# Performance work log

Measured on AMD Instinct MI355X. Metric: run time of the kernel, lower is better.

Reference implementation:

```python
import jax, jax.numpy as jnp
import numpy as np

N = 100000          # nodes
E = 800000          # directed edges (before self-loops)
IN_C = 3
HID = 48            # out_channels per head
HEADS = 4
NUM_LAYERS = 3
NEG_SLOPE = 0.2     # PyG GATv2Conv default negative_slope


def setup_inputs() -> dict:
    key = jax.random.key(0)
    ks = iter(jax.random.split(key, 64))
    inp = {}
    inp["x"] = jax.random.normal(next(ks), (N, IN_C), dtype=jnp.float32)
    inp["edge_index"] = jax.random.randint(next(ks), (2, E), 0, N, dtype=jnp.int32)
    dins = [IN_C] + [HID] * (NUM_LAYERS - 1)
    for l, din in enumerate(dins):
        s = 1.0 / np.sqrt(din)
        inp[f"Wl{l}"] = (jax.random.normal(next(ks), (din, HEADS * HID)) * s).astype(jnp.float32)
        inp[f"bl{l}"] = jnp.zeros((HEADS * HID,), jnp.float32)
        inp[f"Wr{l}"] = (jax.random.normal(next(ks), (din, HEADS * HID)) * s).astype(jnp.float32)
        inp[f"br{l}"] = jnp.zeros((HEADS * HID,), jnp.float32)
        inp[f"att{l}"] = (jax.random.normal(next(ks), (HEADS, HID)) / np.sqrt(HID)).astype(jnp.float32)
        inp[f"b{l}"] = jnp.zeros((HID,), jnp.float32)
    inp["head_w"] = (jax.random.normal(next(ks), (HID, 1)) / np.sqrt(HID)).astype(jnp.float32)
    inp["head_b"] = jnp.full((1,), 0.1, jnp.float32)
    return inp


def _gatv2_layer(x, src, dst, Wl, bl, Wr, br, att, bias):
    # PyG GATv2Conv, concat=False, share_weights=False, eval mode (no dropout).
    # x: [N, din]; src/dst: [E'] with self-loops appended.
    xl = (x @ Wl + bl).reshape(N, HEADS, HID)   # lin_l(x) -> source features
    xr = (x @ Wr + br).reshape(N, HEADS, HID)   # lin_r(x) -> target features
    e = jax.nn.leaky_relu(xl[src] + xr[dst], NEG_SLOPE)      # [E', H, C]
    logits = jnp.einsum('ehc,hc->eh', e, att)                # [E', H]
    # numerically stable per-destination-node softmax over incoming edges
    m = jax.ops.segment_max(logits, dst, num_segments=N)     # [N, H]
    ex = jnp.exp(logits - m[dst])
    denom = jax.ops.segment_sum(ex, dst, num_segments=N)     # [N, H]
    alpha = ex / (denom[dst] + 1e-16)                        # [E', H]
    out = jax.ops.segment_sum(xl[src] * alpha[..., None], dst, num_segments=N)  # [N, H, C]
    return out.mean(axis=1) + bias                           # concat=False -> mean over heads, + bias


def reference(x, edge_index, Wl0, bl0, Wr0, br0, att0, b0,
              Wl1, bl1, Wr1, br1, att1, b1,
              Wl2, bl2, Wr2, br2, att2, b2, head_w, head_b):
    loop = jnp.arange(N, dtype=edge_index.dtype)
    src = jnp.concatenate([edge_index[0], loop])  # add_self_loops=True (PyG default)
    dst = jnp.concatenate([edge_index[1], loop])
    params = [(Wl0, bl0, Wr0, br0, att0, b0),
              (Wl1, bl1, Wr1, br1, att1, b1),
              (Wl2, bl2, Wr2, br2, att2, b2)]
    for p in params:
        x = jax.nn.elu(_gatv2_layer(x, src, dst, *p))  # F.elu; dropout is identity in eval
    out = (x @ head_w + head_b)[:, 0]                  # Linear head, squeeze(-1)
    return jax.nn.softplus(out)                        # output_activation='softplus'
```

## Files before the change

### kernel.cpp

```cpp
#include <hip/hip_runtime.h>
#include <math.h>

#define NN 100000
#define NPAD 100032
#define EE 800000
#define NHEADS 4
#define HID 48
#define FDIM (NHEADS * HID)
#define ROWB 384
#define KPAD 64
#define SCAN_CHUNK 2048
#define NBLK ((NN + SCAN_CHUNK - 1) / SCAN_CHUNK)

typedef unsigned int uint;
typedef unsigned short ushort;

#if __has_builtin(__builtin_amdgcn_exp2f)
#define EXP2(x) __builtin_amdgcn_exp2f(x)
#else
#define EXP2(x) exp2f(x)
#endif

struct U3 { uint x, y, z; };

typedef __attribute__((ext_vector_type(8))) short s16x8;
typedef __attribute__((ext_vector_type(4))) float f32x4;


__global__ void hist_k(const int* __restrict__ ei, int* __restrict__ cnt) {
    int e = blockIdx.x * blockDim.x + threadIdx.x;
    if (e >= EE) return;
    atomicAdd(&cnt[ei[EE + e]], 1);
}

__global__ void scan1_k(const int* __restrict__ cnt, int* __restrict__ rowptr,
                        int* __restrict__ bsum) {
    __shared__ int lds[256];
    int b = blockIdx.x, t = threadIdx.x;
    int base = b * SCAN_CHUNK + t * 8;
    int v[8], s = 0;
#pragma unroll
    for (int i = 0; i < 8; i++) { v[i] = (base + i < NN) ? cnt[base + i] : 0; s += v[i]; }
    lds[t] = s;
    __syncthreads();
    for (int off = 1; off < 256; off <<= 1) {
        int val = (t >= off) ? lds[t - off] : 0;
        __syncthreads();
        lds[t] += val;
        __syncthreads();
    }
    if (t == 255) bsum[b] = lds[255];
    int run = lds[t] - s;
#pragma unroll
    for (int i = 0; i < 8; i++) {
        if (base + i < NN) rowptr[base + i] = run;
        run += v[i];
    }
}

__global__ void scan2_k(int* __restrict__ bsum) {
    if (threadIdx.x == 0 && blockIdx.x == 0) {
        int acc = 0;
        for (int b = 0; b < NBLK; b++) { int v = bsum[b]; bsum[b] = acc; acc += v; }
    }
}

__global__ void scan3_k(int* __restrict__ rowptr, const int* __restrict__ bsum) {
    int i = blockIdx.x * blockDim.x + threadIdx.x;
    if (i < NN) rowptr[i] += bsum[i / SCAN_CHUNK];
}

__global__ void scatter_k(const int* __restrict__ ei, const int* __restrict__ rowptr,
                          int* __restrict__ fill, int* __restrict__ esrc) {
    int e = blockIdx.x * blockDim.x + threadIdx.x;
    if (e >= EE) return;
    int d = ei[EE + e];
    int pos = rowptr[d] + atomicAdd(&fill[d], 1);
    esrc[pos] = ei[e];
}


__device__ __forceinline__ uint f2bf(float x) {
    uint u = __float_as_uint(x);
    return (u + 0x7FFFu + ((u >> 16) & 1u)) >> 16;
}
__device__ __forceinline__ float bfl(uint u) { return __uint_as_float(u << 16); }
__device__ __forceinline__ float bfh(uint u) { return __uint_as_float(u & 0xFFFF0000u); }

__global__ void wprep_k(const float* __restrict__ Wl1, const float* __restrict__ Wr1,
                        const float* __restrict__ Wl2, const float* __restrict__ Wr2,
                        ushort* __restrict__ Wt1, ushort* __restrict__ Wt2) {
    int t = blockIdx.x * blockDim.x + threadIdx.x;
    if (t >= 2 * KPAD * 384) return;
    int l = t / (KPAD * 384);
    int rem = t - l * (KPAD * 384);
    int k = rem / 384;
    int c = rem - k * 384;
    int cc = (c >= 192) ? c - 192 : c;
    const float* W = (l == 0) ? (c < 192 ? Wl1 : Wr1) : (c < 192 ? Wl2 : Wr2);
    float v = (k < 48) ? W[k * FDIM + cc] : 0.0f;
    uint hi = f2bf(v);
    float lo = v - bfl(hi);
    uint lob = f2bf(lo);
    ushort* Wt = (l == 0) ? Wt1 : Wt2;
    Wt[c * KPAD + k] = (ushort)hi;
    Wt[384 * KPAD + c * KPAD + k] = (ushort)lob;
}

__launch_bounds__(192)
__global__ void gemm2_k(const float* __restrict__ x,
                        const float* __restrict__ Wl, const float* __restrict__ bl,
                        const float* __restrict__ Wr, const float* __restrict__ br,
                        uint* __restrict__ xlb, uint* __restrict__ xrb) {
    const int DIN = 3;
    __shared__ float xs[32][53];
    int t = threadIdx.x;
    int f4 = t % 48, nb = t / 48;
    int node0 = blockIdx.x * 32;

    for (int idx = t; idx < 32 * DIN; idx += 192) {
        int n = idx / DIN, k = idx - n * DIN;
        xs[n][k] = x[(size_t)(node0 + n) * DIN + k];
    }
    __syncthreads();

    float4 accl[8], accr[8];
    {
        float4 bl4 = *(const float4*)(bl + f4 * 4);
        float4 br4 = *(const float4*)(br + f4 * 4);
#pragma unroll
        for (int r = 0; r < 8; r++) { accl[r] = bl4; accr[r] = br4; }
    }

#pragma unroll
    for (int k = 0; k < DIN; k++) {
        float4 wl4 = *(const float4*)(Wl + k * FDIM + f4 * 4);
        float4 wr4 = *(const float4*)(Wr + k * FDIM + f4 * 4);
#pragma unroll
        for (int r = 0; r < 8; r++) {
            float xv = xs[nb * 8 + r][k];
            accl[r].x = fmaf(xv, wl4.x, accl[r].x);
            accl[r].y = fmaf(xv, wl4.y, accl[r].y);
            accl[r].z = fmaf(xv, wl4.z, accl[r].z);
            accl[r].w = fmaf(xv, wl4.w, accl[r].w);
            accr[r].x = fmaf(xv, wr4.x, accr[r].x);
            accr[r].y = fmaf(xv, wr4.y, accr[r].y);
            accr[r].z = fmaf(xv, wr4.z, accr[r].z);
            accr[r].w = fmaf(xv, wr4.w, accr[r].w);
        }
    }

#pragma unroll
    for (int r = 0; r < 8; r++) {
        size_t n = (size_t)node0 + nb * 8 + r;
        uint2 pl, pr;
        pl.x = f2bf(accl[r].x) | (f2bf(accl[r].y) << 16);
        pl.y = f2bf(accl[r].z) | (f2bf(accl[r].w) << 16);
        pr.x = f2bf(accr[r].x) | (f2bf(accr[r].y) << 16);
        pr.y = f2bf(accr[r].z) | (f2bf(accr[r].w) << 16);
        *(uint2*)((char*)xlb + n * ROWB + f4 * 8) = pl;
        *(uint2*)((char*)xrb + n * ROWB + f4 * 8) = pr;
    }
}

__launch_bounds__(256)
__global__ void gemm_mfma_k(const ushort* __restrict__ xbf,
                            const ushort* __restrict__ Wt,
                            const float* __restrict__ bl, const float* __restrict__ br,
                            ushort* __restrict__ xlb, ushort* __restrict__ xrb) {
    __shared__ ushort cs[64 * 96];
    int cg = blockIdx.x & 3;
    int n0 = (blockIdx.x >> 2) * 64;
    int wave = threadIdx.x >> 6, lane = threadIdx.x & 63;
    int l15 = lane & 15, l16 = lane >> 4;
    int arow = n0 + wave * 16 + l15;
    int k8 = l16 * 8;

    const ushort* ap = xbf + (size_t)arow * KPAD + k8;
    s16x8 a0 = *(const s16x8*)(ap);
    s16x8 a1 = *(const s16x8*)(ap + 32);

    f32x4 acc[6];
#pragma unroll
    for (int ct = 0; ct < 6; ct++) {
        int cglob = cg * 96 + ct * 16 + l15;
        float bv = (cglob < 192) ? bl[cglob] : br[cglob - 192];
        acc[ct] = (f32x4){bv, bv, bv, bv};
        const ushort* bp = Wt + (size_t)cglob * KPAD + k8;
        s16x8 bh0 = *(const s16x8*)(bp);
        s16x8 bh1 = *(const s16x8*)(bp + 32);
        s16x8 bl0 = *(const s16x8*)(bp + 384 * KPAD);
        s16x8 bl1 = *(const s16x8*)(bp + 384 * KPAD + 32);
        acc[ct] = __builtin_amdgcn_mfma_f32_16x16x32_bf16(a0, bh0, acc[ct], 0, 0, 0);
        acc[ct] = __builtin_amdgcn_mfma_f32_16x16x32_bf16(a1, bh1, acc[ct], 0, 0, 0);
        acc[ct] = __builtin_amdgcn_mfma_f32_16x16x32_bf16(a0, bl0, acc[ct], 0, 0, 0);
        acc[ct] = __builtin_amdgcn_mfma_f32_16x16x32_bf16(a1, bl1, acc[ct], 0, 0, 0);
    }

#pragma unroll
    for (int ct = 0; ct < 6; ct++) {
#pragma unroll
        for (int r = 0; r < 4; r++) {
            int row = wave * 16 + l16 * 4 + r;
            cs[row * 96 + ct * 16 + l15] = (ushort)f2bf(acc[ct][r]);
        }
    }
    __syncthreads();

    int colbase = cg * 96;
    ushort* outm = (colbase < 192) ? xlb : xrb;
    int cb = (colbase >= 192) ? colbase - 192 : colbase;
#pragma unroll
    for (int i = 0; i < 3; i++) {
        int idx = threadIdx.x + i * 256;
        int row = idx / 12, q = idx - row * 12;
        int node = n0 + row;
        if (node < NN) {
            uint4 v = *(const uint4*)(&cs[row * 96 + q * 8]);
            *(uint4*)(outm + (size_t)node * FDIM + cb + q * 8) = v;
        }
    }
}

template <int CTRL>
__device__ __forceinline__ float dpp_add(float x) {
    int v = __builtin_amdgcn_update_dpp(0, __float_as_int(x), CTRL, 0xF, 0xF, true);
    return x + __int_as_float(v);
}
__device__ __forceinline__ float red8(float x) {
    x = dpp_add<0x141>(x);
    x = dpp_add<0x04E>(x);
    x = dpp_add<0x0B1>(x);
    return x;
}

#define GAT_PAIR(CU, VALID)                                                      \
    {                                                                            \
        float ca0 = bfl(CU.x), ca1 = bfh(CU.x), ca2 = bfl(CU.y);                 \
        float ca3 = bfh(CU.y), ca4 = bfl(CU.z), ca5 = bfh(CU.z);                 \
        float t0 = ca0 + r0; t0 = fmaxf(t0, 0.2f * t0);                          \
        float t1 = ca1 + r1; t1 = fmaxf(t1, 0.2f * t1);                          \
        float t2 = ca2 + r2; t2 = fmaxf(t2, 0.2f * t2);                          \
        float t3 = ca3 + r3; t3 = fmaxf(t3, 0.2f * t3);                          \
        float t4 = ca4 + r4; t4 = fmaxf(t4, 0.2f * t4);                          \
        float t5 = ca5 + r5; t5 = fmaxf(t5, 0.2f * t5);                          \
        float l = red8(fmaf(t0, w0, fmaf(t1, w1, fmaf(t2, w2,                    \
                       fmaf(t3, w3, fmaf(t4, w4, t5 * w5))))));                  \
        float mn = (VALID) ? fmaxf(m, l) : m;                                    \
        float p = (VALID) ? EXP2(l - mn) : 0.0f;                                 \
        float c = EXP2(m - mn);                                                  \
        s = fmaf(s, c, p);                                                       \
        o0 = fmaf(o0, c, p * ca0);                                               \
        o1 = fmaf(o1, c, p * ca1);                                               \
        o2 = fmaf(o2, c, p * ca2);                                               \
        o3 = fmaf(o3, c, p * ca3);                                               \
        o4 = fmaf(o4, c, p * ca4);                                               \
        o5 = fmaf(o5, c, p * ca5);                                               \
        m = mn;                                                                  \
    }

__global__ void gat_node_k(const uint* __restrict__ xlb, const uint* __restrict__ xrb,
                           const int* __restrict__ rowptr, const int* __restrict__ cnt,
                           const int* __restrict__ esrc, const float* __restrict__ att,
                           const float* __restrict__ bias,
                           ushort* __restrict__ xbf_out, float* __restrict__ xf_out) {
    int wid = (blockIdx.x * blockDim.x + threadIdx.x) >> 6;
    int lane = threadIdx.x & 63;
    if (wid >= NN) return;
    int d = wid;
    int half = lane >> 5;
    int hb = lane & 31;
    int h = hb >> 3;
    int j = hb & 7;
    int boff = h * 96 + j * 12;
    int half4 = half << 2;

    const float LOG2E = 1.4426950408889634f;
    const float* ap = att + h * HID + j * 6;
    float w0 = ap[0] * LOG2E, w1 = ap[1] * LOG2E, w2 = ap[2] * LOG2E;
    float w3 = ap[3] * LOG2E, w4 = ap[4] * LOG2E, w5 = ap[5] * LOG2E;

    const char* xlc = (const char*)xlb;
    const char* xrc = (const char*)xrb;

    U3 ur = *(const U3*)(xrc + (size_t)d * ROWB + boff);
    float r0 = bfl(ur.x), r1 = bfh(ur.x), r2 = bfl(ur.y);
    float r3 = bfh(ur.y), r4 = bfl(ur.z), r5 = bfh(ur.z);

    U3 us = *(const U3*)(xlc + (size_t)d * ROWB + boff);
    float a0 = bfl(us.x), a1 = bfh(us.x), a2 = bfl(us.y);
    float a3 = bfh(us.y), a4 = bfl(us.z), a5 = bfh(us.z);
    float v0 = a0 + r0; v0 = fmaxf(v0, 0.2f * v0);
    float v1 = a1 + r1; v1 = fmaxf(v1, 0.2f * v1);
    float v2 = a2 + r2; v2 = fmaxf(v2, 0.2f * v2);
    float v3 = a3 + r3; v3 = fmaxf(v3, 0.2f * v3);
    float v4 = a4 + r4; v4 = fmaxf(v4, 0.2f * v4);
    float v5 = a5 + r5; v5 = fmaxf(v5, 0.2f * v5);
    float lself = red8(fmaf(v0, w0, fmaf(v1, w1, fmaf(v2, w2,
                       fmaf(v3, w3, fmaf(v4, w4, v5 * w5))))));

    float m = half ? -3.0e38f : lself;
    float s = half ? 0.0f : 1.0f;
    float o0 = half ? 0.f : a0, o1 = half ? 0.f : a1, o2 = half ? 0.f : a2;
    float o3 = half ? 0.f : a3, o4 = half ? 0.f : a4, o5 = half ? 0.f : a5;

    int start = rowptr[d], deg = cnt[d];

    for (int cb = 0; cb < deg; cb += 64) {
        int rem = deg - cb; if (rem > 64) rem = 64;
        int my_src = 0;
        if (lane < rem) my_src = esrc[start + cb + lane];
        int npairs = (rem + 1) >> 1;

        int sA = __builtin_amdgcn_ds_bpermute(half4, my_src);
        int sB = __builtin_amdgcn_ds_bpermute(8 + half4, my_src);
        U3 cur = *(const U3*)(xlc + (uint)sA * (uint)ROWB + (uint)boff);

        for (int i = 0; i < npairs - 1; i++) {
            U3 nxt = *(const U3*)(xlc + (uint)sB * (uint)ROWB + (uint)boff);
            sB = __builtin_amdgcn_ds_bpermute(((i + 2) << 3) + half4, my_src);
            GAT_PAIR(cur, true);
            cur = nxt;
        }
        {
            bool valid = (((npairs - 1) << 1) + half) < rem;
            GAT_PAIR(cur, valid);
        }
    }

    float m2 = __shfl_xor(m, 32);
    float s2 = __shfl_xor(s, 32);
    float mn = fmaxf(m, m2);
    float c1 = EXP2(m - mn), c2 = EXP2(m2 - mn);
    float sm = fmaf(s, c1, s2 * c2);
    float inv = 1.0f / (sm + 1e-16f);
    float q0 = fmaf(o0, c1, __shfl_xor(o0, 32) * c2) * inv;
    float q1 = fmaf(o1, c1, __shfl_xor(o1, 32) * c2) * inv;
    float q2 = fmaf(o2, c1, __shfl_xor(o2, 32) * c2) * inv;
    float q3 = fmaf(o3, c1, __shfl_xor(o3, 32) * c2) * inv;
    float q4 = fmaf(o4, c1, __shfl_xor(o4, 32) * c2) * inv;
    float q5 = fmaf(o5, c1, __shfl_xor(o5, 32) * c2) * inv;

    q0 += __shfl_xor(q0, 8); q0 += __shfl_xor(q0, 16);
    q1 += __shfl_xor(q1, 8); q1 += __shfl_xor(q1, 16);
    q2 += __shfl_xor(q2, 8); q2 += __shfl_xor(q2, 16);
    q3 += __shfl_xor(q3, 8); q3 += __shfl_xor(q3, 16);
    q4 += __shfl_xor(q4, 8); q4 += __shfl_xor(q4, 16);
    q5 += __shfl_xor(q5, 8); q5 += __shfl_xor(q5, 16);

    if (lane < 8) {
        const float* bp = bias + j * 6;
        float y0 = fmaf(q0, 0.25f, bp[0]);
        float y1 = fmaf(q1, 0.25f, bp[1]);
        float y2 = fmaf(q2, 0.25f, bp[2]);
        float y3 = fmaf(q3, 0.25f, bp[3]);
        float y4 = fmaf(q4, 0.25f, bp[4]);
        float y5 = fmaf(q5, 0.25f, bp[5]);
        y0 = y0 > 0.f ? y0 : (EXP2(y0 * LOG2E) - 1.0f);
        y1 = y1 > 0.f ? y1 : (EXP2(y1 * LOG2E) - 1.0f);
        y2 = y2 > 0.f ? y2 : (EXP2(y2 * LOG2E) - 1.0f);
        y3 = y3 > 0.f ? y3 : (EXP2(y3 * LOG2E) - 1.0f);
        y4 = y4 > 0.f ? y4 : (EXP2(y4 * LOG2E) - 1.0f);
        y5 = y5 > 0.f ? y5 : (EXP2(y5 * LOG2E) - 1.0f);
        if (xbf_out) {
            U3 pk;
            pk.x = f2bf(y0) | (f2bf(y1) << 16);
            pk.y = f2bf(y2) | (f2bf(y3) << 16);
            pk.z = f2bf(y4) | (f2bf(y5) << 16);
            *(U3*)(xbf_out + (size_t)d * KPAD + j * 6) = pk;
        }
        if (xf_out) {
            float* qo = xf_out + (size_t)d * HID + j * 6;
            *(float2*)(qo) = make_float2(y0, y1);
            *(float2*)(qo + 2) = make_float2(y2, y3);
            *(float2*)(qo + 4) = make_float2(y4, y5);
        }
    }
}

__global__ void head_k(const float* __restrict__ x, const float* __restrict__ w,
                       const float* __restrict__ hb, float* __restrict__ out) {
    int n = blockIdx.x * blockDim.x + threadIdx.x;
    if (n >= NN) return;
    const float* p = x + (size_t)n * HID;
    float acc = 0.f;
#pragma unroll
    for (int c = 0; c < HID; c++) acc = fmaf(p[c], w[c], acc);
    acc += hb[0];
    out[n] = fmaxf(acc, 0.f) + log1pf(expf(-fabsf(acc)));
}

static inline int cdiv(long a, long b) { return (int)((a + b - 1) / b); }

extern "C" void kernel_launch(void* const* d_in, const int* in_sizes, int n_in,
                              void* d_out, int out_size, void* d_ws, size_t ws_size,
                              hipStream_t stream) {
    const float* x0 = (const float*)d_in[0];
    const int* ei = (const int*)d_in[1];
    const float* Wl[3] = {(const float*)d_in[2], (const float*)d_in[8], (const float*)d_in[14]};
    const float* bl[3] = {(const float*)d_in[3], (const float*)d_in[9], (const float*)d_in[15]};
    const float* Wr[3] = {(const float*)d_in[4], (const float*)d_in[10], (const float*)d_in[16]};
    const float* br[3] = {(const float*)d_in[5], (const float*)d_in[11], (const float*)d_in[17]};
    const float* att[3] = {(const float*)d_in[6], (const float*)d_in[12], (const float*)d_in[18]};
    const float* bb[3] = {(const float*)d_in[7], (const float*)d_in[13], (const float*)d_in[19]};
    const float* hw = (const float*)d_in[20];
    const float* hb = (const float*)d_in[21];

    char* ws = (char*)d_ws;
    uint* xlb = (uint*)ws;      ws += (size_t)NN * ROWB;
    uint* xrb = (uint*)ws;      ws += (size_t)NN * ROWB;
    float* bufA = (float*)ws;   ws += (size_t)NN * HID * 4;
    ushort* xbf = (ushort*)ws;  ws += (size_t)NPAD * KPAD * 2;
    ushort* Wt1 = (ushort*)ws;  ws += (size_t)2 * 384 * KPAD * 2;
    ushort* Wt2 = (ushort*)ws;  ws += (size_t)2 * 384 * KPAD * 2;
    int* rowptr = (int*)ws;     ws += (size_t)NN * 4;
    int* cnt = (int*)ws;        ws += (size_t)NN * 4;
    int* fill = (int*)ws;       ws += (size_t)NN * 4;
    int* esrc = (int*)ws;       ws += (size_t)EE * 4;
    int* bsum = (int*)ws;       ws += (size_t)NBLK * 4;

    hipMemsetAsync(cnt, 0, (size_t)NN * 4, stream);
    hipMemsetAsync(fill, 0, (size_t)NN * 4, stream);
    hipMemsetAsync(xbf, 0, (size_t)NPAD * KPAD * 2, stream);
    wprep_k<<<cdiv(2 * KPAD * 384, 256), 256, 0, stream>>>(Wl[1], Wr[1], Wl[2], Wr[2], Wt1, Wt2);
    hist_k<<<cdiv(EE, 256), 256, 0, stream>>>(ei, cnt);
    scan1_k<<<NBLK, 256, 0, stream>>>(cnt, rowptr, bsum);
    scan2_k<<<1, 64, 0, stream>>>(bsum);
    scan3_k<<<cdiv(NN, 256), 256, 0, stream>>>(rowptr, bsum);
    scatter_k<<<cdiv(EE, 256), 256, 0, stream>>>(ei, rowptr, fill, esrc);

    const int GAT_GRID = cdiv((long)NN * 64, 256);
    const int MFMA_GRID = cdiv(NN, 64) * 4;

    gemm2_k<<<NN / 32, 192, 0, stream>>>(x0, Wl[0], bl[0], Wr[0], br[0], xlb, xrb);
    gat_node_k<<<GAT_GRID, 256, 0, stream>>>(xlb, xrb, rowptr, cnt, esrc, att[0], bb[0],
                                             xbf, (float*)nullptr);
    gemm_mfma_k<<<MFMA_GRID, 256, 0, stream>>>(xbf, Wt1, bl[1], br[1],
                                               (ushort*)xlb, (ushort*)xrb);
    gat_node_k<<<GAT_GRID, 256, 0, stream>>>(xlb, xrb, rowptr, cnt, esrc, att[1], bb[1],
                                             xbf, (float*)nullptr);
    gemm_mfma_k<<<MFMA_GRID, 256, 0, stream>>>(xbf, Wt2, bl[2], br[2],
                                               (ushort*)xlb, (ushort*)xrb);
    gat_node_k<<<GAT_GRID, 256, 0, stream>>>(xlb, xrb, rowptr, cnt, esrc, att[2], bb[2],
                                             (ushort*)nullptr, bufA);

    head_k<<<cdiv(NN, 256), 256, 0, stream>>>(bufA, hw, hb, (float*)d_out);
}
```

Before: 485.9 us.

## Fuse head projection into last GAT layer and tile MFMA GEMM over multiple node tiles

The final linear head and softplus are folded into the last gat_node_k, using a DPP reduction across the 8 lanes holding a node's features. This removes the fp32 intermediate buffer write/read and one kernel launch. The MFMA GEMM now keeps the weight fragments in registers and loops over four 64-node tiles per block, prefetching the next A tile. It uses per-wave LDS staging without __syncthreads, which cuts redundant weight loads but raises register pressure and reduces the grid size.

```diff
diff --git a/kernel.cpp b/kernel.cpp
--- a/kernel.cpp
+++ b/kernel.cpp
@@ -2,13 +2,14 @@
 #include <math.h>
 
 #define NN 100000
-#define NPAD 100032
+#define NPAD 100096
 #define EE 800000
 #define NHEADS 4
 #define HID 48
 #define FDIM (NHEADS * HID)
 #define ROWB 384
 #define KPAD 64
+#define TLES 4
 #define SCAN_CHUNK 2048
 #define NBLK ((NN + SCAN_CHUNK - 1) / SCAN_CHUNK)
 
@@ -168,57 +169,68 @@
                             const ushort* __restrict__ Wt,
                             const float* __restrict__ bl, const float* __restrict__ br,
                             ushort* __restrict__ xlb, ushort* __restrict__ xrb) {
-    __shared__ ushort cs[64 * 96];
+    __shared__ ushort cs[4][16][104];
     int cg = blockIdx.x & 3;
-    int n0 = (blockIdx.x >> 2) * 64;
+    int n0 = (blockIdx.x >> 2) * (64 * TLES);
     int wave = threadIdx.x >> 6, lane = threadIdx.x & 63;
     int l15 = lane & 15, l16 = lane >> 4;
-    int arow = n0 + wave * 16 + l15;
     int k8 = l16 * 8;
 
-    const ushort* ap = xbf + (size_t)arow * KPAD + k8;
-    s16x8 a0 = *(const s16x8*)(ap);
-    s16x8 a1 = *(const s16x8*)(ap + 32);
-
-    f32x4 acc[6];
+    s16x8 vbh0[6], vbh1[6], vbl0[6], vbl1[6];
+    float bv[6];
 #pragma unroll
     for (int ct = 0; ct < 6; ct++) {
         int cglob = cg * 96 + ct * 16 + l15;
-        float bv = (cglob < 192) ? bl[cglob] : br[cglob - 192];
-        acc[ct] = (f32x4){bv, bv, bv, bv};
+        bv[ct] = (cglob < 192) ? bl[cglob] : br[cglob - 192];
         const ushort* bp = Wt + (size_t)cglob * KPAD + k8;
-        s16x8 bh0 = *(const s16x8*)(bp);
-        s16x8 bh1 = *(const s16x8*)(bp + 32);
-        s16x8 bl0 = *(const s16x8*)(bp + 384 * KPAD);
-        s16x8 bl1 = *(const s16x8*)(bp + 384 * KPAD + 32);
-        acc[ct] = __builtin_amdgcn_mfma_f32_16x16x32_bf16(a0, bh0, acc[ct], 0, 0, 0);
-        acc[ct] = __builtin_amdgcn_mfma_f32_16x16x32_bf16(a1, bh1, acc[ct], 0, 0, 0);
-        acc[ct] = __builtin_amdgcn_mfma_f32_16x16x32_bf16(a0, bl0, acc[ct], 0, 0, 0);
-        acc[ct] = __builtin_amdgcn_mfma_f32_16x16x32_bf16(a1, bl1, acc[ct], 0, 0, 0);
-    }
-
-#pragma unroll
-    for (int ct = 0; ct < 6; ct++) {
-#pragma unroll
-        for (int r = 0; r < 4; r++) {
-            int row = wave * 16 + l16 * 4 + r;
-            cs[row * 96 + ct * 16 + l15] = (ushort)f2bf(acc[ct][r]);
-        }
-    }
-    __syncthreads();
+        vbh0[ct] = *(const s16x8*)(bp);
+        vbh1[ct] = *(const s16x8*)(bp + 32);
+        vbl0[ct] = *(const s16x8*)(bp + 384 * KPAD);
+        vbl1[ct] = *(const s16x8*)(bp + 384 * KPAD + 32);
+    }
 
     int colbase = cg * 96;
     ushort* outm = (colbase < 192) ? xlb : xrb;
     int cb = (colbase >= 192) ? colbase - 192 : colbase;
-#pragma unroll
-    for (int i = 0; i < 3; i++) {
-        int idx = threadIdx.x + i * 256;
-        int row = idx / 12, q = idx - row * 12;
-        int node = n0 + row;
-        if (node < NN) {
-            uint4 v = *(const uint4*)(&cs[row * 96 + q * 8]);
-            *(uint4*)(outm + (size_t)node * FDIM + cb + q * 8) = v;
-        }
+
+    const ushort* ap = xbf + (size_t)(n0 + wave * 16 + l15) * KPAD + k8;
+    s16x8 a0 = *(const s16x8*)(ap);
+    s16x8 a1 = *(const s16x8*)(ap + 32);
+
+#pragma unroll
+    for (int t = 0; t < TLES; t++) {
+        s16x8 na0, na1;
+        if (t + 1 < TLES) {
+            const ushort* np = ap + (size_t)(t + 1) * 64 * KPAD;
+            na0 = *(const s16x8*)(np);
+            na1 = *(const s16x8*)(np + 32);
+        }
+        f32x4 acc[6];
+#pragma unroll
+        for (int ct = 0; ct < 6; ct++) {
+            acc[ct] = (f32x4){bv[ct], bv[ct], bv[ct], bv[ct]};
+            acc[ct] = __builtin_amdgcn_mfma_f32_16x16x32_bf16(a0, vbh0[ct], acc[ct], 0, 0, 0);
+            acc[ct] = __builtin_amdgcn_mfma_f32_16x16x32_bf16(a1, vbh1[ct], acc[ct], 0, 0, 0);
+            acc[ct] = __builtin_amdgcn_mfma_f32_16x16x32_bf16(a0, vbl0[ct], acc[ct], 0, 0, 0);
+            acc[ct] = __builtin_amdgcn_mfma_f32_16x16x32_bf16(a1, vbl1[ct], acc[ct], 0, 0, 0);
+        }
+#pragma unroll
+        for (int ct = 0; ct < 6; ct++)
+#pragma unroll
+            for (int r = 0; r < 4; r++)
+                cs[wave][l16 * 4 + r][ct * 16 + l15] = (ushort)f2bf(acc[ct][r]);
+        int nb0 = n0 + t * 64 + wave * 16;
+#pragma unroll
+        for (int i = 0; i < 3; i++) {
+            int idx = lane + i * 64;
+            int row = idx / 12, q = idx - row * 12;
+            int node = nb0 + row;
+            if (node < NN) {
+                uint4 v = *(const uint4*)(&cs[wave][row][q * 8]);
+                *(uint4*)(outm + (size_t)node * FDIM + cb + q * 8) = v;
+            }
+        }
+        if (t + 1 < TLES) { a0 = na0; a1 = na1; }
     }
 }
 
@@ -263,7 +275,9 @@
                            const int* __restrict__ rowptr, const int* __restrict__ cnt,
                            const int* __restrict__ esrc, const float* __restrict__ att,
                            const float* __restrict__ bias,
-                           ushort* __restrict__ xbf_out, float* __restrict__ xf_out) {
+                           ushort* __restrict__ xbf_out,
+                           const float* __restrict__ headw, const float* __restrict__ headb,
+                           float* __restrict__ out) {
     int wid = (blockIdx.x * blockDim.x + threadIdx.x) >> 6;
     int lane = threadIdx.x & 63;
     if (wid >= NN) return;
@@ -362,32 +376,23 @@
         y3 = y3 > 0.f ? y3 : (EXP2(y3 * LOG2E) - 1.0f);
         y4 = y4 > 0.f ? y4 : (EXP2(y4 * LOG2E) - 1.0f);
         y5 = y5 > 0.f ? y5 : (EXP2(y5 * LOG2E) - 1.0f);
-        if (xbf_out) {
+        if (headw) {
+            const float* hp = headw + j * 6;
+            float pd = fmaf(y0, hp[0], fmaf(y1, hp[1], fmaf(y2, hp[2],
+                       fmaf(y3, hp[3], fmaf(y4, hp[4], y5 * hp[5])))));
+            pd = red8(pd);
+            if (j == 0) {
+                float acc = pd + headb[0];
+                out[d] = fmaxf(acc, 0.f) + log1pf(expf(-fabsf(acc)));
+            }
+        } else {
             U3 pk;
             pk.x = f2bf(y0) | (f2bf(y1) << 16);
             pk.y = f2bf(y2) | (f2bf(y3) << 16);
             pk.z = f2bf(y4) | (f2bf(y5) << 16);
             *(U3*)(xbf_out + (size_t)d * KPAD + j * 6) = pk;
         }
-        if (xf_out) {
-            float* qo = xf_out + (size_t)d * HID + j * 6;
-            *(float2*)(qo) = make_float2(y0, y1);
-            *(float2*)(qo + 2) = make_float2(y2, y3);
-            *(float2*)(qo + 4) = make_float2(y4, y5);
-        }
-    }
-}
-
-__global__ void head_k(const float* __restrict__ x, const float* __restrict__ w,
-                       const float* __restrict__ hb, float* __restrict__ out) {
-    int n = blockIdx.x * blockDim.x + threadIdx.x;
-    if (n >= NN) return;
-    const float* p = x + (size_t)n * HID;
-    float acc = 0.f;
-#pragma unroll
-    for (int c = 0; c < HID; c++) acc = fmaf(p[c], w[c], acc);
-    acc += hb[0];
-    out[n] = fmaxf(acc, 0.f) + log1pf(expf(-fabsf(acc)));
+    }
 }
 
 static inline int cdiv(long a, long b) { return (int)((a + b - 1) / b); }
@@ -409,7 +414,6 @@
     char* ws = (char*)d_ws;
     uint* xlb = (uint*)ws;      ws += (size_t)NN * ROWB;
     uint* xrb = (uint*)ws;      ws += (size_t)NN * ROWB;
-    float* bufA = (float*)ws;   ws += (size_t)NN * HID * 4;
     ushort* xbf = (ushort*)ws;  ws += (size_t)NPAD * KPAD * 2;
     ushort* Wt1 = (ushort*)ws;  ws += (size_t)2 * 384 * KPAD * 2;
     ushort* Wt2 = (ushort*)ws;  ws += (size_t)2 * 384 * KPAD * 2;
@@ -430,19 +434,17 @@
     scatter_k<<<cdiv(EE, 256), 256, 0, stream>>>(ei, rowptr, fill, esrc);
 
     const int GAT_GRID = cdiv((long)NN * 64, 256);
-    const int MFMA_GRID = cdiv(NN, 64) * 4;
+    const int MFMA_GRID = cdiv(NN, 64 * TLES) * 4;
 
     gemm2_k<<<NN / 32, 192, 0, stream>>>(x0, Wl[0], bl[0], Wr[0], br[0], xlb, xrb);
     gat_node_k<<<GAT_GRID, 256, 0, stream>>>(xlb, xrb, rowptr, cnt, esrc, att[0], bb[0],
-                                             xbf, (float*)nullptr);
+                                             xbf, nullptr, nullptr, nullptr);
     gemm_mfma_k<<<MFMA_GRID, 256, 0, stream>>>(xbf, Wt1, bl[1], br[1],
                                                (ushort*)xlb, (ushort*)xrb);
     gat_node_k<<<GAT_GRID, 256, 0, stream>>>(xlb, xrb, rowptr, cnt, esrc, att[1], bb[1],
-                                             xbf, (float*)nullptr);
+                                             xbf, nullptr, nullptr, nullptr);
     gemm_mfma_k<<<MFMA_GRID, 256, 0, stream>>>(xbf, Wt2, bl[2], br[2],
                                                (ushort*)xlb, (ushort*)xrb);
     gat_node_k<<<GAT_GRID, 256, 0, stream>>>(xlb, xrb, rowptr, cnt, esrc, att[2], bb[2],
-                                             (ushort*)nullptr, bufA);
-
-    head_k<<<cdiv(NN, 256), 256, 0, stream>>>(bufA, hw, hb, (float*)d_out);
-}
+                                             nullptr, hw, hb, (float*)d_out);
+}
```

After: 424.7 us. 1.14x faster.
